# Kernel tuning notes

Measured on AMD Instinct MI355X. Metric: run time of the kernel, lower is better.

The kernel has to match this reference:

```python
import jax, jax.numpy as jnp
import numpy as np

B, S, D, C, K, V = 128, 512, 300, 300, 3, 30000  # batch, seq, embed=hidden, capsule, categories, vocab
PAD_INDEX = 0
SQUASH_EPS = 1e-8
MASK_NEG = -1e9


def squash(x, axis=-1):
    # v * (|v|^2 / (1+|v|^2)) / |v|
    sq = jnp.sum(x * x, axis=axis, keepdims=True)
    return (sq / (1.0 + sq)) * x / jnp.sqrt(sq + SQUASH_EPS)


def setup_inputs() -> dict:
    key = jax.random.key(0)
    ks = jax.random.split(key, 11)
    return {
        "sentence": jax.random.randint(ks[0], (B, S), 0, V),
        "aspect": jax.random.randint(ks[1], (B,), 0, V),
        "category_alpha": jax.random.uniform(ks[2], (B, S), dtype=jnp.float32),
        "embed": jax.random.normal(ks[3], (V, D), dtype=jnp.float32) * 0.02,
        "W_s": jax.random.normal(ks[4], (D, C), dtype=jnp.float32) * 0.02,
        "b_s": jnp.zeros((C,), dtype=jnp.float32),
        "W_a": jax.random.normal(ks[5], (D, C), dtype=jnp.float32) * 0.02,
        "b_a": jnp.zeros((C,), dtype=jnp.float32),
        "W_att": jax.random.normal(ks[6], (C, C), dtype=jnp.float32) * 0.02,
        "guide_capsule": jax.random.normal(ks[7], (K, C), dtype=jnp.float32) * 0.02,
        "guide_weight": jax.random.normal(ks[8], (C, C), dtype=jnp.float32) * 0.02,
        "scale": jnp.asarray(5.0, dtype=jnp.float32),
    }


def reference(sentence, aspect, category_alpha, embed, W_s, b_s, W_a, b_a,
              W_att, guide_capsule, guide_weight, scale):
    mask = sentence != PAD_INDEX                      # [B,S]
    emb = embed[sentence]                             # [B,S,D]
    asp = embed[aspect]                               # [B,D]

    # element_wise_mul (vectorized): per-token alpha weighting
    caml = emb * category_alpha[..., None]            # [B,S,D]
    cavl = jnp.sum(caml, axis=1)                      # [B,D] (unused in non-Cav path)
    del cavl

    # _sentence_encode stand-in (abstract in source): alpha-weighted embeddings
    sent_enc = caml                                   # [B,S,hidden=D]

    primary = squash(sent_enc @ W_s + b_s)            # [B,S,C]
    aspect_capsule = squash(asp @ W_a + b_a)          # [B,C]

    # bilinear attention weights with padding mask, softmax over sequence
    scores = jnp.einsum('bsc,cd,bd->bs', primary, W_att, aspect_capsule)
    scores = jnp.where(mask, scores, MASK_NEG)
    norm_weight = jax.nn.softmax(scores, axis=-1)     # [B,S]

    # capsule-guided routing
    guide = squash(guide_capsule)                     # [K,C]
    gm = jnp.einsum('bsc,cd,kd->bsk', primary, guide_weight, guide)
    gm = jax.nn.softmax(gm, axis=-1) * norm_weight[..., None] * scale
    category_capsule = squash(jnp.einsum('bsk,bsc->bkc', gm, primary))  # [B,K,C]

    return jnp.sqrt(jnp.sum(category_capsule * category_capsule, axis=-1))  # [B,K]
```

## Files before the change

kernel.cpp:

```cpp
#include <hip/hip_runtime.h>

#define NV 30000
#define NB 128
#define NS 512
#define ND 300
#define NC 300
#define CP 304
#define KP 320
#define EP 304
#define MASK_NEG -1e9f
#define SQ_EPS 1e-8f

typedef __attribute__((ext_vector_type(4))) float f32x4;
typedef __attribute__((ext_vector_type(8))) __bf16 bf16x8;

__device__ __forceinline__ unsigned short f2bf(float x){
  unsigned int u = __float_as_uint(x);
  u += 0x7FFFu + ((u >> 16) & 1u);
  return (unsigned short)(u >> 16);
}
__device__ __forceinline__ float bf2f(unsigned short h){
  return __uint_as_float(((unsigned int)h) << 16);
}

__device__ __forceinline__ float bsum512(float v, float* red, int tid){
  red[tid] = v; __syncthreads();
  float s = 0.f;
  if (tid < 64){
    s = red[tid]+red[tid+64]+red[tid+128]+red[tid+192]
      + red[tid+256]+red[tid+320]+red[tid+384]+red[tid+448];
    #pragma unroll
    for (int off = 32; off > 0; off >>= 1) s += __shfl_xor(s, off);
    if (tid == 0) red[0] = s;
  }
  __syncthreads();
  s = red[0];
  __syncthreads();
  return s;
}

__device__ __forceinline__ float bmax512(float v, float* red, int tid){
  red[tid] = v; __syncthreads();
  float s = MASK_NEG;
  if (tid < 64){
    s = red[tid];
    #pragma unroll
    for (int o = 64; o < 512; o += 64) s = fmaxf(s, red[tid+o]);
    #pragma unroll
    for (int off = 32; off > 0; off >>= 1) s = fmaxf(s, __shfl_xor(s, off));
    if (tid == 0) red[0] = s;
  }
  __syncthreads();
  s = red[0];
  __syncthreads();
  return s;
}

__global__ __launch_bounds__(512) void kprep(
    const float* __restrict__ Ws, const float* __restrict__ Watt,
    const float* __restrict__ Gw, const float* __restrict__ bs,
    const float* __restrict__ gcap, const int* __restrict__ aspect,
    const float* __restrict__ embed, const float* __restrict__ Wa,
    const float* __restrict__ ba,
    unsigned short* __restrict__ wt, float* __restrict__ bsp,
    unsigned short* __restrict__ BMT)
{
  int bid = blockIdx.x, tid = threadIdx.x;
  int lane = tid & 63, w = tid >> 6;
  __shared__ float sh[64*65];
  float* aspL = sh;
  float* capL = sh + 320;
  float* red  = sh + 640;

  if (bid < 25) {
    float (*t)[65] = (float(*)[65])sh;
    int kt = bid / 5, nt = bid - kt*5;
    #pragma unroll
    for (int i = 0; i < 8; i++){
      int idx = i*512 + tid;
      int r = idx >> 6, c = idx & 63;
      int gk = kt*64 + r, gn = nt*64 + c;
      t[r][c] = (gk < ND && gn < NC) ? Ws[gk*NC + gn] : 0.f;
    }
    __syncthreads();
    #pragma unroll
    for (int i = 0; i < 8; i++){
      int idx = i*512 + tid;
      int n = idx >> 6, k = idx & 63;
      wt[(nt*64 + n)*KP + kt*64 + k] = f2bf(t[k][n]);
    }
  } else if (bid == 25) {
    float bv = 0.f;
    if (tid < 320){
      bv = (tid < NC) ? bs[tid] : 0.f;
      bsp[tid] = bv;
      BMT[131*KP + tid] = f2bf(bv);
    }
    for (int i = tid; i < 28*KP; i += 512) BMT[132*KP + i] = 0;
  } else if (bid < 154) {
    int b = bid - 26;
    int a = aspect[b];
    if (tid < 320) aspL[tid] = (tid < ND) ? embed[(size_t)a*ND + tid] : 0.f;
    __syncthreads();
    int c = tid;
    float p0=0.f,p1=0.f,p2=0.f,p3=0.f,p4=0.f,p5=0.f;
    if (c < NC){
      for (int d = 0; d < 300; d += 6){
        p0 += Wa[(d+0)*NC + c]*aspL[d+0];
        p1 += Wa[(d+1)*NC + c]*aspL[d+1];
        p2 += Wa[(d+2)*NC + c]*aspL[d+2];
        p3 += Wa[(d+3)*NC + c]*aspL[d+3];
        p4 += Wa[(d+4)*NC + c]*aspL[d+4];
        p5 += Wa[(d+5)*NC + c]*aspL[d+5];
      }
    }
    float z = (c < NC) ? (ba[c] + ((p0+p1)+(p2+p3)+(p4+p5))) : 0.f;
    float sq = bsum512((c < NC) ? z*z : 0.f, red, tid);
    float ssv = (sq/(1.f+sq))/sqrtf(sq + SQ_EPS);
    if (tid < 320) capL[tid] = (c < NC) ? z*ssv : 0.f;
    __syncthreads();
    for (int cc = w; cc < NC; cc += 8){
      const float* wr = Watt + (size_t)cc*NC;
      float acc = 0.f;
      #pragma unroll
      for (int j = 0; j < 5; j++){
        int d = j*64 + lane;
        float wv = (d < ND) ? wr[d] : 0.f;
        acc += wv*capL[d];
      }
      #pragma unroll
      for (int off = 32; off > 0; off >>= 1) acc += __shfl_xor(acc, off);
      if (lane == 0) BMT[(size_t)b*KP + cc] = f2bf(acc);
    }
    if (tid < 20) BMT[(size_t)b*KP + 300 + tid] = 0;
  } else {
    int k = bid - 154;
    if (tid < 320) aspL[tid] = (tid < NC) ? gcap[k*NC + tid] : 0.f;
    __syncthreads();
    float g = (tid < 320) ? aspL[tid] : 0.f;
    float sq = bsum512((tid < NC) ? g*g : 0.f, red, tid);
    float ssv = (sq/(1.f+sq))/sqrtf(sq + SQ_EPS);
    if (tid < 320) capL[tid] = g*ssv;
    __syncthreads();
    for (int cc = w; cc < NC; cc += 8){
      const float* wr = Gw + (size_t)cc*NC;
      float acc = 0.f;
      #pragma unroll
      for (int j = 0; j < 5; j++){
        int d = j*64 + lane;
        float wv = (d < ND) ? wr[d] : 0.f;
        acc += wv*capL[d];
      }
      #pragma unroll
      for (int off = 32; off > 0; off >>= 1) acc += __shfl_xor(acc, off);
      if (lane == 0) BMT[(size_t)(128+k)*KP + cc] = f2bf(acc);
    }
    if (tid < 20) BMT[(size_t)(128+k)*KP + 300 + tid] = 0;
  }
}

#define BM 64
#define BKT 64
#define LDK 72
#define LDE 328
__global__ __launch_bounds__(512) void k1f(
    const float* __restrict__ embed, const unsigned short* __restrict__ wt,
    const unsigned short* __restrict__ BMT, const float* __restrict__ bsp,
    unsigned short* __restrict__ E, float* __restrict__ EtT,
    float* __restrict__ ETS)
{
  __shared__ unsigned short lds_a[BM*LDK];
  __shared__ unsigned short lds_b[KP*LDK];
  __shared__ float e2part[4][BM];
  int tid = threadIdx.x;
  int lane = tid & 63, wid = tid >> 6;
  int bid = blockIdx.x;
  bool special = (bid == (NV + BM - 1)/BM);
  int rowbase = special ? NV : bid * BM;
  unsigned short* et = lds_b;

  if (!special){
    int wrow = wid >> 2, wcol = wid & 3;
    f32x4 acc[2][5];
    f32x4 zero = {0.f,0.f,0.f,0.f};
    #pragma unroll
    for (int m = 0; m < 2; m++)
      #pragma unroll
      for (int n = 0; n < 5; n++) acc[m][n] = zero;

    for (int k0 = 0; k0 < KP; k0 += BKT){
      #pragma unroll
      for (int r = 0; r < 2; r++){
        int id = r*512 + tid;
        int row = id >> 4, k4 = (id & 15) << 2;
        int gk = k0 + k4, grow = rowbase + row;
        float4 v = {0.f,0.f,0.f,0.f};
        if (grow < NV && gk < ND) v = *(const float4*)(embed + (size_t)grow*ND + gk);
        unsigned int lo = (unsigned int)f2bf(v.x) | ((unsigned int)f2bf(v.y) << 16);
        unsigned int hi = (unsigned int)f2bf(v.z) | ((unsigned int)f2bf(v.w) << 16);
        uint2 pk; pk.x = lo; pk.y = hi;
        *(uint2*)(lds_a + row*LDK + k4) = pk;
      }
      #pragma unroll
      for (int r = 0; r < 5; r++){
        int id = r*512 + tid;
        int n = id >> 3, koff = (id & 7) << 3;
        uint4 v = *(const uint4*)(wt + n*KP + k0 + koff);
        *(uint4*)(lds_b + n*LDK + koff) = v;
      }
      __syncthreads();
      #pragma unroll
      for (int kk = 0; kk < BKT; kk += 32){
        bf16x8 af[2], bfr[5];
        int kidx = kk + (lane >> 4)*8;
        int arow = wrow*32 + (lane & 15);
        int brow = wcol*80 + (lane & 15);
        #pragma unroll
        for (int m = 0; m < 2; m++) af[m] = *(const bf16x8*)(lds_a + (arow + m*16)*LDK + kidx);
        #pragma unroll
        for (int n = 0; n < 5; n++) bfr[n] = *(const bf16x8*)(lds_b + (brow + n*16)*LDK + kidx);
        #pragma unroll
        for (int m = 0; m < 2; m++)
          #pragma unroll
          for (int n = 0; n < 5; n++)
            acc[m][n] = __builtin_amdgcn_mfma_f32_16x16x32_bf16(af[m], bfr[n], acc[m][n], 0, 0, 0);
      }
      __syncthreads();
    }
    int colb = wcol*80 + (lane & 15);
    int rowb0 = wrow*32 + ((lane >> 4) << 2);
    #pragma unroll
    for (int m = 0; m < 2; m++)
      #pragma unroll
      for (int n = 0; n < 5; n++)
        #pragma unroll
        for (int j = 0; j < 4; j++){
          int rloc = rowb0 + m*16 + j;
          int row = rowbase + rloc;
          int col = colb + n*16;
          unsigned short h = f2bf(acc[m][n][j]);
          if (row < NV && col < EP) E[(size_t)row*EP + col] = h;
          et[rloc*LDE + col] = h;
        }
    #pragma unroll
    for (int m = 0; m < 2; m++)
      #pragma unroll
      for (int j = 0; j < 4; j++){
        float p = 0.f;
        #pragma unroll
        for (int n = 0; n < 5; n++){ float t = acc[m][n][j]; p += t*t; }
        #pragma unroll
        for (int off = 1; off < 16; off <<= 1) p += __shfl_xor(p, off);
        if ((lane & 15) == 0)
          e2part[wcol][rowb0 + m*16 + j] = p;
      }
  } else {
    for (int i = tid; i < 64*LDE; i += 512) et[i] = 0;
    if (tid < 320) et[tid] = f2bf(bsp[tid]);
  }
  __syncthreads();
  if (!special && tid < BM){
    int grow = rowbase + tid;
    if (grow < NV){
      float s = e2part[0][tid] + e2part[1][tid] + e2part[2][tid] + e2part[3][tid];
      ETS[(size_t)grow*8 + 4] = s;
    }
  }
  int wr2 = wid >> 1, wc2 = wid & 1;
  f32x4 acc2[5];
  f32x4 z2 = {0.f,0.f,0.f,0.f};
  #pragma unroll
  for (int n = 0; n < 5; n++) acc2[n] = z2;
  #pragma unroll 2
  for (int kk = 0; kk < KP; kk += 32){
    int kidx = kk + (lane >> 4)*8;
    bf16x8 a2 = *(const bf16x8*)(et + (wr2*16 + (lane & 15))*LDE + kidx);
    #pragma unroll
    for (int n = 0; n < 5; n++){
      bf16x8 b2 = *(const bf16x8*)(BMT + (size_t)(wc2*80 + n*16 + (lane & 15))*KP + kidx);
      acc2[n] = __builtin_amdgcn_mfma_f32_16x16x32_bf16(a2, b2, acc2[n], 0, 0, 0);
    }
  }
  int colb2 = wc2*80 + (lane & 15);
  int rowb2 = rowbase + wr2*16 + ((lane >> 4) << 2);
  int rlim = special ? (NV + 1) : NV;
  #pragma unroll
  for (int n = 0; n < 5; n++)
    #pragma unroll
    for (int j = 0; j < 4; j++){
      int row = rowb2 + j;
      int col = colb2 + n*16;
      if (row < rlim){
        if (col < 128)      EtT[(size_t)row*128 + col] = acc2[n][j];
        else if (col < 132) ETS[(size_t)row*8 + (col - 128)] = acc2[n][j];
      }
    }
}

__global__ __launch_bounds__(512) void k45(
    const int* __restrict__ sentence, const float* __restrict__ alpha,
    const float* __restrict__ scale_p, const unsigned short* __restrict__ E,
    const float* __restrict__ EtT, const float* __restrict__ ETS,
    const float* __restrict__ bsp, float* __restrict__ out)
{
  int b = blockIdx.x, tid = threadIdx.x;
  int lane = tid & 63, w = tid >> 6;
  __shared__ float red[512];
  __shared__ float cfs[NS*3];
  __shared__ int toksh[NS];
  __shared__ float cap8[8][3][CP];
  __shared__ float vall[3*CP];

  int idx = (b << 9) + tid;
  int tok = sentence[idx];
  float al = alpha[idx];
  toksh[tid] = tok;
  float et  = EtT[(size_t)tok*128 + b];
  float4 eg = *(const float4*)(ETS + (size_t)tok*8);
  float e2v = ETS[(size_t)tok*8 + 4];
  float bst = EtT[(size_t)NV*128 + b];
  float4 brs = *(const float4*)(ETS + (size_t)NV*8);

  float sq  = al*al*e2v + 2.f*al*eg.w + brs.w;
  float ssv = (sq/(1.f+sq))/sqrtf(sq + SQ_EPS);
  float scv = (tok != 0) ? ssv*(al*et + bst) : MASK_NEG;
  float u0 = ssv*(al*eg.x + brs.x);
  float u1 = ssv*(al*eg.y + brs.y);
  float u2 = ssv*(al*eg.z + brs.z);

  float m = bmax512(scv, red, tid);
  float e = expf(scv - m);
  float Z = bsum512(e, red, tid);
  float nw = e / Z;
  float mk = fmaxf(u0, fmaxf(u1, u2));
  float e0 = expf(u0-mk), e1 = expf(u1-mk), e2 = expf(u2-mk);
  float wf = nw * scale_p[0] / (e0+e1+e2);
  float w0 = e0*wf, w1 = e1*wf, w2 = e2*wf;
  float ca = ssv * al;
  cfs[tid*3+0] = w0*ca; cfs[tid*3+1] = w1*ca; cfs[tid*3+2] = w2*ca;
  float sb0 = bsum512(w0*ssv, red, tid);
  float sb1 = bsum512(w1*ssv, red, tid);
  float sb2 = bsum512(w2*ssv, red, tid);
  __syncthreads();

  f32x4 A0 = {0.f,0.f,0.f,0.f}, A1 = A0, A2 = A0, R0 = A0, R1 = A0, R2 = A0;
  int c0 = lane << 2;
  int c1 = 256 + (lane << 2);
  bool rem = lane < 12;
  int base = w << 6;
  #pragma unroll 4
  for (int i = 0; i < 64; i++){
    int s = base + i;
    int t = toksh[s];
    const unsigned short* erow = E + (size_t)t*EP;
    uint2 ev = *(const uint2*)(erow + c0);
    float cf0 = cfs[s*3+0], cf1 = cfs[s*3+1], cf2 = cfs[s*3+2];
    f32x4 y;
    y[0] = bf2f((unsigned short)(ev.x & 0xffffu));
    y[1] = bf2f((unsigned short)(ev.x >> 16));
    y[2] = bf2f((unsigned short)(ev.y & 0xffffu));
    y[3] = bf2f((unsigned short)(ev.y >> 16));
    A0 += cf0*y; A1 += cf1*y; A2 += cf2*y;
    if (rem){
      uint2 ev2 = *(const uint2*)(erow + c1);
      f32x4 yr;
      yr[0] = bf2f((unsigned short)(ev2.x & 0xffffu));
      yr[1] = bf2f((unsigned short)(ev2.x >> 16));
      yr[2] = bf2f((unsigned short)(ev2.y & 0xffffu));
      yr[3] = bf2f((unsigned short)(ev2.y >> 16));
      R0 += cf0*yr; R1 += cf1*yr; R2 += cf2*yr;
    }
  }
  *(f32x4*)&cap8[w][0][c0] = A0;
  *(f32x4*)&cap8[w][1][c0] = A1;
  *(f32x4*)&cap8[w][2][c0] = A2;
  if (rem){
    *(f32x4*)&cap8[w][0][c1] = R0;
    *(f32x4*)&cap8[w][1][c1] = R1;
    *(f32x4*)&cap8[w][2][c1] = R2;
  }
  __syncthreads();
  float sbk[3] = {sb0, sb1, sb2};
  for (int p = tid; p < 3*CP; p += 512){
    int k = p / CP, c = p - k*CP;
    float v = sbk[k]*bsp[c];
    #pragma unroll
    for (int w8 = 0; w8 < 8; w8++) v += cap8[w8][k][c];
    vall[p] = v;
  }
  __syncthreads();
  #pragma unroll
  for (int k = 0; k < 3; k++){
    float x = 0.f;
    if (tid < CP){ float t = vall[k*CP + tid]; x = t*t; }
    float s = bsum512(x, red, tid);
    if (tid == 0){
      out[b*3 + k] = (s/(1.f+s))*sqrtf(s)/sqrtf(s + SQ_EPS);
    }
  }
}

extern "C" void kernel_launch(void* const* d_in, const int* in_sizes, int n_in,
                              void* d_out, int out_size, void* d_ws, size_t ws_size,
                              hipStream_t stream)
{
  (void)in_sizes; (void)n_in; (void)out_size; (void)ws_size;
  const int*   sentence = (const int*)d_in[0];
  const int*   aspect   = (const int*)d_in[1];
  const float* alpha    = (const float*)d_in[2];
  const float* embed    = (const float*)d_in[3];
  const float* Ws       = (const float*)d_in[4];
  const float* bs       = (const float*)d_in[5];
  const float* Wa       = (const float*)d_in[6];
  const float* ba       = (const float*)d_in[7];
  const float* Watt     = (const float*)d_in[8];
  const float* gcap     = (const float*)d_in[9];
  const float* gw       = (const float*)d_in[10];
  const float* scale    = (const float*)d_in[11];
  float* out = (float*)d_out;

  char* w = (char*)d_ws;
  auto alloc = [&](size_t bytes)->char*{
    char* p = w; w += (bytes + 255) & ~(size_t)255; return p;
  };
  unsigned short* WT  = (unsigned short*)alloc((size_t)KP*KP*2);
  unsigned short* E   = (unsigned short*)alloc((size_t)NV*EP*2);
  float* ETT = (float*)alloc((size_t)(NV+1)*128*4);
  float* ETS = (float*)alloc((size_t)(NV+1)*8*4);
  float* BSP = (float*)alloc(320*4);
  unsigned short* BMT = (unsigned short*)alloc((size_t)160*KP*2);

  kprep<<<157, 512, 0, stream>>>(Ws, Watt, gw, bs, gcap, aspect, embed, Wa, ba,
                                 WT, BSP, BMT);
  k1f<<<(NV + BM - 1)/BM + 1, 512, 0, stream>>>(embed, WT, BMT, BSP, E, ETT, ETS);
  k45<<<NB, 512, 0, stream>>>(sentence, alpha, scale, E, ETT, ETS, BSP, out);
}
```

Baseline: 112.3 us.

## Fold attention/guide projections into combined weight and defer Ws projection to end

New measurement: 120.4 us. 7.2% more time.

```diff
diff --git a/kernel.cpp b/kernel.cpp
--- a/kernel.cpp
+++ b/kernel.cpp
@@ -7,20 +7,21 @@
 #define NC 300
 #define CP 304
 #define KP 320
-#define EP 304
 #define MASK_NEG -1e9f
 #define SQ_EPS 1e-8f
 
 typedef __attribute__((ext_vector_type(4))) float f32x4;
 typedef __attribute__((ext_vector_type(8))) __bf16 bf16x8;
 
-__device__ __forceinline__ unsigned short f2bf(float x){
+__device__ __forceinline__ unsigned int f2bfu(float x){
   unsigned int u = __float_as_uint(x);
   u += 0x7FFFu + ((u >> 16) & 1u);
-  return (unsigned short)(u >> 16);
-}
-__device__ __forceinline__ float bf2f(unsigned short h){
-  return __uint_as_float(((unsigned int)h) << 16);
+  return u >> 16;
+}
+__device__ __forceinline__ unsigned short f2bf(float x){ return (unsigned short)f2bfu(x); }
+
+__device__ __forceinline__ int swzk(int row, int k){
+  return (k & ~0x38) | (((((k >> 3) & 7) ^ (row & 7)) & 7) << 3);
 }
 
 __device__ __forceinline__ float bsum512(float v, float* red, int tid){
@@ -62,15 +63,15 @@
     const float* __restrict__ gcap, const int* __restrict__ aspect,
     const float* __restrict__ embed, const float* __restrict__ Wa,
     const float* __restrict__ ba,
-    unsigned short* __restrict__ wt, float* __restrict__ bsp,
-    unsigned short* __restrict__ BMT)
+    unsigned short* __restrict__ WTC, float* __restrict__ BC)
 {
   int bid = blockIdx.x, tid = threadIdx.x;
   int lane = tid & 63, w = tid >> 6;
   __shared__ float sh[64*65];
-  float* aspL = sh;
+  float* vecL = sh;
   float* capL = sh + 320;
-  float* red  = sh + 640;
+  float* tL   = sh + 640;
+  float* red  = sh + 960;
 
   if (bid < 25) {
     float (*t)[65] = (float(*)[65])sh;
@@ -87,40 +88,56 @@
     for (int i = 0; i < 8; i++){
       int idx = i*512 + tid;
       int n = idx >> 6, k = idx & 63;
-      wt[(nt*64 + n)*KP + kt*64 + k] = f2bf(t[k][n]);
+      int row = nt*64 + n, gk = kt*64 + k;
+      WTC[row*KP + swzk(row, gk)] = f2bf(t[k][n]);
     }
   } else if (bid == 25) {
-    float bv = 0.f;
-    if (tid < 320){
-      bv = (tid < NC) ? bs[tid] : 0.f;
-      bsp[tid] = bv;
-      BMT[131*KP + tid] = f2bf(bv);
-    }
-    for (int i = tid; i < 28*KP; i += 512) BMT[132*KP + i] = 0;
-  } else if (bid < 154) {
-    int b = bid - 26;
+    for (int i = tid; i < 60*KP; i += 512) WTC[452*KP + i] = 0;
+    float bv = (tid < NC) ? bs[tid] : 0.f;
+    float s2 = bsum512(bv*bv, red, tid);
+    if (tid == 0) BC[131] = s2;
+  } else if (bid == 26) {
+    if (tid < 320) vecL[tid] = (tid < NC) ? bs[tid] : 0.f;
+    __syncthreads();
+    for (int d = w; d < 320; d += 8){
+      float acc = 0.f;
+      if (d < ND){
+        const float* wr = Ws + (size_t)d*NC;
+        #pragma unroll
+        for (int j = 0; j < 5; j++){
+          int c = j*64 + lane;
+          float wv = (c < NC) ? wr[c] : 0.f;
+          acc += wv*vecL[c];
+        }
+        #pragma unroll
+        for (int off = 32; off > 0; off >>= 1) acc += __shfl_xor(acc, off);
+      }
+      if (lane == 0) WTC[451*KP + swzk(451, d)] = (d < ND) ? f2bf(acc) : (unsigned short)0;
+    }
+  } else if (bid < 155) {
+    int b = bid - 27;
     int a = aspect[b];
-    if (tid < 320) aspL[tid] = (tid < ND) ? embed[(size_t)a*ND + tid] : 0.f;
-    __syncthreads();
-    int c = tid;
-    float p0=0.f,p1=0.f,p2=0.f,p3=0.f,p4=0.f,p5=0.f;
-    if (c < NC){
+    if (tid < 320) vecL[tid] = (tid < ND) ? embed[(size_t)a*ND + tid] : 0.f;
+    __syncthreads();
+    float z = 0.f;
+    if (tid < NC){
+      float p0=0.f,p1=0.f,p2=0.f,p3=0.f,p4=0.f,p5=0.f;
       for (int d = 0; d < 300; d += 6){
-        p0 += Wa[(d+0)*NC + c]*aspL[d+0];
-        p1 += Wa[(d+1)*NC + c]*aspL[d+1];
-        p2 += Wa[(d+2)*NC + c]*aspL[d+2];
-        p3 += Wa[(d+3)*NC + c]*aspL[d+3];
-        p4 += Wa[(d+4)*NC + c]*aspL[d+4];
-        p5 += Wa[(d+5)*NC + c]*aspL[d+5];
-      }
-    }
-    float z = (c < NC) ? (ba[c] + ((p0+p1)+(p2+p3)+(p4+p5))) : 0.f;
-    float sq = bsum512((c < NC) ? z*z : 0.f, red, tid);
+        p0 += Wa[(d+0)*NC + tid]*vecL[d+0];
+        p1 += Wa[(d+1)*NC + tid]*vecL[d+1];
+        p2 += Wa[(d+2)*NC + tid]*vecL[d+2];
+        p3 += Wa[(d+3)*NC + tid]*vecL[d+3];
+        p4 += Wa[(d+4)*NC + tid]*vecL[d+4];
+        p5 += Wa[(d+5)*NC + tid]*vecL[d+5];
+      }
+      z = ba[tid] + ((p0+p1)+(p2+p3)+(p4+p5));
+    }
+    float sq = bsum512((tid < NC) ? z*z : 0.f, red, tid);
     float ssv = (sq/(1.f+sq))/sqrtf(sq + SQ_EPS);
-    if (tid < 320) capL[tid] = (c < NC) ? z*ssv : 0.f;
-    __syncthreads();
-    for (int cc = w; cc < NC; cc += 8){
-      const float* wr = Watt + (size_t)cc*NC;
+    if (tid < 320) capL[tid] = (tid < NC) ? z*ssv : 0.f;
+    __syncthreads();
+    for (int c = w; c < NC; c += 8){
+      const float* wr = Watt + (size_t)c*NC;
       float acc = 0.f;
       #pragma unroll
       for (int j = 0; j < 5; j++){
@@ -130,20 +147,39 @@
       }
       #pragma unroll
       for (int off = 32; off > 0; off >>= 1) acc += __shfl_xor(acc, off);
-      if (lane == 0) BMT[(size_t)b*KP + cc] = f2bf(acc);
-    }
-    if (tid < 20) BMT[(size_t)b*KP + 300 + tid] = 0;
+      if (lane == 0) tL[c] = acc;
+    }
+    __syncthreads();
+    if (tid < 20) tL[300 + tid] = 0.f;
+    float bst = bsum512((tid < NC) ? bs[tid]*tL[tid] : 0.f, red, tid);
+    if (tid == 0) BC[b] = bst;
+    int row = 320 + b;
+    for (int d = w; d < 320; d += 8){
+      float acc = 0.f;
+      if (d < ND){
+        const float* wr = Ws + (size_t)d*NC;
+        #pragma unroll
+        for (int j = 0; j < 5; j++){
+          int c = j*64 + lane;
+          float wv = (c < NC) ? wr[c] : 0.f;
+          acc += wv*tL[c];
+        }
+        #pragma unroll
+        for (int off = 32; off > 0; off >>= 1) acc += __shfl_xor(acc, off);
+      }
+      if (lane == 0) WTC[row*KP + swzk(row, d)] = (d < ND) ? f2bf(acc) : (unsigned short)0;
+    }
   } else {
-    int k = bid - 154;
-    if (tid < 320) aspL[tid] = (tid < NC) ? gcap[k*NC + tid] : 0.f;
-    __syncthreads();
-    float g = (tid < 320) ? aspL[tid] : 0.f;
+    int k = bid - 155;
+    if (tid < 320) vecL[tid] = (tid < NC) ? gcap[k*NC + tid] : 0.f;
+    __syncthreads();
+    float g = (tid < 320) ? vecL[tid] : 0.f;
     float sq = bsum512((tid < NC) ? g*g : 0.f, red, tid);
     float ssv = (sq/(1.f+sq))/sqrtf(sq + SQ_EPS);
     if (tid < 320) capL[tid] = g*ssv;
     __syncthreads();
-    for (int cc = w; cc < NC; cc += 8){
-      const float* wr = Gw + (size_t)cc*NC;
+    for (int c = w; c < NC; c += 8){
+      const float* wr = Gw + (size_t)c*NC;
       float acc = 0.f;
       #pragma unroll
       for (int j = 0; j < 5; j++){
@@ -153,222 +189,218 @@
       }
       #pragma unroll
       for (int off = 32; off > 0; off >>= 1) acc += __shfl_xor(acc, off);
-      if (lane == 0) BMT[(size_t)(128+k)*KP + cc] = f2bf(acc);
-    }
-    if (tid < 20) BMT[(size_t)(128+k)*KP + 300 + tid] = 0;
-  }
-}
-
-#define BM 64
-#define BKT 64
+      if (lane == 0) tL[c] = acc;
+    }
+    __syncthreads();
+    if (tid < 20) tL[300 + tid] = 0.f;
+    float bsg = bsum512((tid < NC) ? bs[tid]*tL[tid] : 0.f, red, tid);
+    if (tid == 0) BC[128 + k] = bsg;
+    int row = 448 + k;
+    for (int d = w; d < 320; d += 8){
+      float acc = 0.f;
+      if (d < ND){
+        const float* wr = Ws + (size_t)d*NC;
+        #pragma unroll
+        for (int j = 0; j < 5; j++){
+          int c = j*64 + lane;
+          float wv = (c < NC) ? wr[c] : 0.f;
+          acc += wv*tL[c];
+        }
+        #pragma unroll
+        for (int off = 32; off > 0; off >>= 1) acc += __shfl_xor(acc, off);
+      }
+      if (lane == 0) WTC[row*KP + swzk(row, d)] = (d < ND) ? f2bf(acc) : (unsigned short)0;
+    }
+  }
+}
+
 #define LDK 72
-#define LDE 328
-__global__ __launch_bounds__(512) void k1f(
-    const float* __restrict__ embed, const unsigned short* __restrict__ wt,
-    const unsigned short* __restrict__ BMT, const float* __restrict__ bsp,
-    unsigned short* __restrict__ E, float* __restrict__ EtT,
-    float* __restrict__ ETS)
+__global__ __launch_bounds__(512, 4) void k1f(
+    const float* __restrict__ embed, const unsigned short* __restrict__ WTC,
+    float* __restrict__ EtT, float* __restrict__ ETS)
 {
-  __shared__ unsigned short lds_a[BM*LDK];
-  __shared__ unsigned short lds_b[KP*LDK];
-  __shared__ float e2part[4][BM];
-  int tid = threadIdx.x;
-  int lane = tid & 63, wid = tid >> 6;
+  __shared__ unsigned short lds_a[64*LDK];
+  __shared__ unsigned short lds_b[512*64];
+  __shared__ float e2part[3][64];
+  int tid = threadIdx.x, lane = tid & 63, wid = tid >> 6;
+  int wrow = wid >> 2, wcol = wid & 3;
+  int rowbase = blockIdx.x * 64;
+  f32x4 acc[2][8];
+  f32x4 zero = {0.f,0.f,0.f,0.f};
+  #pragma unroll
+  for (int m = 0; m < 2; m++)
+    #pragma unroll
+    for (int n = 0; n < 8; n++) acc[m][n] = zero;
+
+  float4 pa[2];
+  auto loadA = [&](int k0){
+    #pragma unroll
+    for (int r = 0; r < 2; r++){
+      int id = r*512 + tid;
+      int row = id >> 4, k4 = (id & 15) << 2;
+      int grow = rowbase + row, gk = k0 + k4;
+      float4 v = {0.f,0.f,0.f,0.f};
+      if (grow < NV && gk < ND) v = *(const float4*)(embed + (size_t)grow*ND + gk);
+      pa[r] = v;
+    }
+  };
+  auto writeA = [&](){
+    #pragma unroll
+    for (int r = 0; r < 2; r++){
+      int id = r*512 + tid;
+      int row = id >> 4, k4 = (id & 15) << 2;
+      uint2 pk;
+      pk.x = f2bfu(pa[r].x) | (f2bfu(pa[r].y) << 16);
+      pk.y = f2bfu(pa[r].z) | (f2bfu(pa[r].w) << 16);
+      *(uint2*)(lds_a + row*LDK + k4) = pk;
+    }
+  };
+  auto stageB = [&](int k0){
+    uint4 pb[8];
+    #pragma unroll
+    for (int r = 0; r < 8; r++){
+      int id = r*512 + tid;
+      pb[r] = *(const uint4*)(WTC + (size_t)(id >> 3)*KP + k0 + (id & 7)*8);
+    }
+    #pragma unroll
+    for (int r = 0; r < 8; r++){
+      int id = r*512 + tid;
+      *(uint4*)((char*)lds_b + id*16) = pb[r];
+    }
+  };
+
+  loadA(0);
+  writeA();
+  stageB(0);
+  loadA(64);
+  __syncthreads();
+  for (int step = 0; step < 5; step++){
+    #pragma unroll
+    for (int kk = 0; kk < 64; kk += 32){
+      int kidx = kk + (lane >> 4)*8;
+      bf16x8 af[2];
+      #pragma unroll
+      for (int m = 0; m < 2; m++)
+        af[m] = *(const bf16x8*)(lds_a + (wrow*32 + (lane & 15) + m*16)*LDK + kidx);
+      #pragma unroll
+      for (int n = 0; n < 8; n++){
+        int jrow = wcol*128 + n*16 + (lane & 15);
+        int ch = ((kidx >> 3) & 7) ^ (jrow & 7);
+        bf16x8 bv = *(const bf16x8*)((const char*)lds_b + jrow*128 + ch*16);
+        #pragma unroll
+        for (int m = 0; m < 2; m++)
+          acc[m][n] = __builtin_amdgcn_mfma_f32_16x16x32_bf16(af[m], bv, acc[m][n], 0, 0, 0);
+      }
+    }
+    __syncthreads();
+    if (step < 4){
+      writeA();
+      stageB((step+1)*64);
+      if (step < 3) loadA((step+2)*64);
+      __syncthreads();
+    }
+  }
+
+  int rloc = wrow*32 + ((lane >> 4) << 2);
+  #pragma unroll
+  for (int m = 0; m < 2; m++)
+    #pragma unroll
+    for (int n = 0; n < 8; n++){
+      int col = wcol*128 + n*16 + (lane & 15);
+      #pragma unroll
+      for (int j = 0; j < 4; j++){
+        int grow = rowbase + rloc + m*16 + j;
+        if (grow < NV){
+          if (col >= 320 && col < 448)      EtT[(size_t)grow*128 + (col - 320)] = acc[m][n][j];
+          else if (col >= 448 && col < 452) ETS[(size_t)grow*8 + (col - 448)] = acc[m][n][j];
+        }
+      }
+    }
+  #pragma unroll
+  for (int m = 0; m < 2; m++)
+    #pragma unroll
+    for (int j = 0; j < 4; j++){
+      float p = 0.f;
+      #pragma unroll
+      for (int n = 0; n < 8; n++)
+        if (wcol*128 + n*16 < 320){ float t = acc[m][n][j]; p += t*t; }
+      #pragma unroll
+      for (int off = 1; off < 16; off <<= 1) p += __shfl_xor(p, off);
+      if ((lane & 15) == 0 && wcol < 3) e2part[wcol][rloc + m*16 + j] = p;
+    }
+  __syncthreads();
+  if (tid < 64){
+    int grow = rowbase + tid;
+    if (grow < NV)
+      ETS[(size_t)grow*8 + 4] = e2part[0][tid] + e2part[1][tid] + e2part[2][tid];
+  }
+}
+
+__global__ __launch_bounds__(512) void k45a(
+    const int* __restrict__ sentence, const float* __restrict__ alpha,
+    const float* __restrict__ scale_p, const float* __restrict__ embed,
+    const float* __restrict__ EtT, const float* __restrict__ ETS,
+    const float* __restrict__ BC, float* __restrict__ SBB, float* __restrict__ PRT)
+{
   int bid = blockIdx.x;
-  bool special = (bid == (NV + BM - 1)/BM);
-  int rowbase = special ? NV : bid * BM;
-  unsigned short* et = lds_b;
-
-  if (!special){
-    int wrow = wid >> 2, wcol = wid & 3;
-    f32x4 acc[2][5];
-    f32x4 zero = {0.f,0.f,0.f,0.f};
-    #pragma unroll
-    for (int m = 0; m < 2; m++)
-      #pragma unroll
-      for (int n = 0; n < 5; n++) acc[m][n] = zero;
-
-    for (int k0 = 0; k0 < KP; k0 += BKT){
-      #pragma unroll
-      for (int r = 0; r < 2; r++){
-        int id = r*512 + tid;
-        int row = id >> 4, k4 = (id & 15) << 2;
-        int gk = k0 + k4, grow = rowbase + row;
-        float4 v = {0.f,0.f,0.f,0.f};
-        if (grow < NV && gk < ND) v = *(const float4*)(embed + (size_t)grow*ND + gk);
-        unsigned int lo = (unsigned int)f2bf(v.x) | ((unsigned int)f2bf(v.y) << 16);
-        unsigned int hi = (unsigned int)f2bf(v.z) | ((unsigned int)f2bf(v.w) << 16);
-        uint2 pk; pk.x = lo; pk.y = hi;
-        *(uint2*)(lds_a + row*LDK + k4) = pk;
-      }
-      #pragma unroll
-      for (int r = 0; r < 5; r++){
-        int id = r*512 + tid;
-        int n = id >> 3, koff = (id & 7) << 3;
-        uint4 v = *(const uint4*)(wt + n*KP + k0 + koff);
-        *(uint4*)(lds_b + n*LDK + koff) = v;
-      }
-      __syncthreads();
-      #pragma unroll
-      for (int kk = 0; kk < BKT; kk += 32){
-        bf16x8 af[2], bfr[5];
-        int kidx = kk + (lane >> 4)*8;
-        int arow = wrow*32 + (lane & 15);
-        int brow = wcol*80 + (lane & 15);
-        #pragma unroll
-        for (int m = 0; m < 2; m++) af[m] = *(const bf16x8*)(lds_a + (arow + m*16)*LDK + kidx);
-        #pragma unroll
-        for (int n = 0; n < 5; n++) bfr[n] = *(const bf16x8*)(lds_b + (brow + n*16)*LDK + kidx);
-        #pragma unroll
-        for (int m = 0; m < 2; m++)
-          #pragma unroll
-          for (int n = 0; n < 5; n++)
-            acc[m][n] = __builtin_amdgcn_mfma_f32_16x16x32_bf16(af[m], bfr[n], acc[m][n], 0, 0, 0);
-      }
-      __syncthreads();
-    }
-    int colb = wcol*80 + (lane & 15);
-    int rowb0 = wrow*32 + ((lane >> 4) << 2);
-    #pragma unroll
-    for (int m = 0; m < 2; m++)
-      #pragma unroll
-      for (int n = 0; n < 5; n++)
-        #pragma unroll
-        for (int j = 0; j < 4; j++){
-          int rloc = rowb0 + m*16 + j;
-          int row = rowbase + rloc;
-          int col = colb + n*16;
-          unsigned short h = f2bf(acc[m][n][j]);
-          if (row < NV && col < EP) E[(size_t)row*EP + col] = h;
-          et[rloc*LDE + col] = h;
-        }
-    #pragma unroll
-    for (int m = 0; m < 2; m++)
-      #pragma unroll
-      for (int j = 0; j < 4; j++){
-        float p = 0.f;
-        #pragma unroll
-        for (int n = 0; n < 5; n++){ float t = acc[m][n][j]; p += t*t; }
-        #pragma unroll
-        for (int off = 1; off < 16; off <<= 1) p += __shfl_xor(p, off);
-        if ((lane & 15) == 0)
-          e2part[wcol][rowb0 + m*16 + j] = p;
-      }
-  } else {
-    for (int i = tid; i < 64*LDE; i += 512) et[i] = 0;
-    if (tid < 320) et[tid] = f2bf(bsp[tid]);
-  }
-  __syncthreads();
-  if (!special && tid < BM){
-    int grow = rowbase + tid;
-    if (grow < NV){
-      float s = e2part[0][tid] + e2part[1][tid] + e2part[2][tid] + e2part[3][tid];
-      ETS[(size_t)grow*8 + 4] = s;
-    }
-  }
-  int wr2 = wid >> 1, wc2 = wid & 1;
-  f32x4 acc2[5];
-  f32x4 z2 = {0.f,0.f,0.f,0.f};
-  #pragma unroll
-  for (int n = 0; n < 5; n++) acc2[n] = z2;
-  #pragma unroll 2
-  for (int kk = 0; kk < KP; kk += 32){
-    int kidx = kk + (lane >> 4)*8;
-    bf16x8 a2 = *(const bf16x8*)(et + (wr2*16 + (lane & 15))*LDE + kidx);
-    #pragma unroll
-    for (int n = 0; n < 5; n++){
-      bf16x8 b2 = *(const bf16x8*)(BMT + (size_t)(wc2*80 + n*16 + (lane & 15))*KP + kidx);
-      acc2[n] = __builtin_amdgcn_mfma_f32_16x16x32_bf16(a2, b2, acc2[n], 0, 0, 0);
-    }
-  }
-  int colb2 = wc2*80 + (lane & 15);
-  int rowb2 = rowbase + wr2*16 + ((lane >> 4) << 2);
-  int rlim = special ? (NV + 1) : NV;
-  #pragma unroll
-  for (int n = 0; n < 5; n++)
-    #pragma unroll
-    for (int j = 0; j < 4; j++){
-      int row = rowb2 + j;
-      int col = colb2 + n*16;
-      if (row < rlim){
-        if (col < 128)      EtT[(size_t)row*128 + col] = acc2[n][j];
-        else if (col < 132) ETS[(size_t)row*8 + (col - 128)] = acc2[n][j];
-      }
-    }
-}
-
-__global__ __launch_bounds__(512) void k45(
-    const int* __restrict__ sentence, const float* __restrict__ alpha,
-    const float* __restrict__ scale_p, const unsigned short* __restrict__ E,
-    const float* __restrict__ EtT, const float* __restrict__ ETS,
-    const float* __restrict__ bsp, float* __restrict__ out)
-{
-  int b = blockIdx.x, tid = threadIdx.x;
-  int lane = tid & 63, w = tid >> 6;
+  int b = bid >> 1, hb = bid & 1;
+  int tid = threadIdx.x, lane = tid & 63, w = tid >> 6;
   __shared__ float red[512];
   __shared__ float cfs[NS*3];
   __shared__ int toksh[NS];
   __shared__ float cap8[8][3][CP];
-  __shared__ float vall[3*CP];
 
   int idx = (b << 9) + tid;
   int tok = sentence[idx];
   float al = alpha[idx];
   toksh[tid] = tok;
-  float et  = EtT[(size_t)tok*128 + b];
+  float et = EtT[(size_t)tok*128 + b];
   float4 eg = *(const float4*)(ETS + (size_t)tok*8);
-  float e2v = ETS[(size_t)tok*8 + 4];
-  float bst = EtT[(size_t)NV*128 + b];
-  float4 brs = *(const float4*)(ETS + (size_t)NV*8);
-
-  float sq  = al*al*e2v + 2.f*al*eg.w + brs.w;
+  float e2 = ETS[(size_t)tok*8 + 4];
+  float bst = BC[b];
+  float bsg0 = BC[128], bsg1 = BC[129], bsg2 = BC[130], bs2 = BC[131];
+
+  float sq = al*al*e2 + 2.f*al*eg.w + bs2;
   float ssv = (sq/(1.f+sq))/sqrtf(sq + SQ_EPS);
   float scv = (tok != 0) ? ssv*(al*et + bst) : MASK_NEG;
-  float u0 = ssv*(al*eg.x + brs.x);
-  float u1 = ssv*(al*eg.y + brs.y);
-  float u2 = ssv*(al*eg.z + brs.z);
+  float u0 = ssv*(al*eg.x + bsg0);
+  float u1 = ssv*(al*eg.y + bsg1);
+  float u2 = ssv*(al*eg.z + bsg2);
 
   float m = bmax512(scv, red, tid);
   float e = expf(scv - m);
   float Z = bsum512(e, red, tid);
   float nw = e / Z;
   float mk = fmaxf(u0, fmaxf(u1, u2));
-  float e0 = expf(u0-mk), e1 = expf(u1-mk), e2 = expf(u2-mk);
-  float wf = nw * scale_p[0] / (e0+e1+e2);
-  float w0 = e0*wf, w1 = e1*wf, w2 = e2*wf;
+  float e0 = expf(u0-mk), e1 = expf(u1-mk), e2k = expf(u2-mk);
+  float wf = nw * scale_p[0] / (e0+e1+e2k);
+  float w0 = e0*wf, w1 = e1*wf, w2 = e2k*wf;
   float ca = ssv * al;
   cfs[tid*3+0] = w0*ca; cfs[tid*3+1] = w1*ca; cfs[tid*3+2] = w2*ca;
   float sb0 = bsum512(w0*ssv, red, tid);
   float sb1 = bsum512(w1*ssv, red, tid);
   float sb2 = bsum512(w2*ssv, red, tid);
+  if (hb == 0 && tid == 0){ SBB[b*3+0] = sb0; SBB[b*3+1] = sb1; SBB[b*3+2] = sb2; }
   __syncthreads();
 
   f32x4 A0 = {0.f,0.f,0.f,0.f}, A1 = A0, A2 = A0, R0 = A0, R1 = A0, R2 = A0;
   int c0 = lane << 2;
   int c1 = 256 + (lane << 2);
-  bool rem = lane < 12;
-  int base = w << 6;
+  bool rem = lane < 11;
+  int base = (hb << 8) + (w << 5);
   #pragma unroll 4
-  for (int i = 0; i < 64; i++){
+  for (int i = 0; i < 32; i++){
     int s = base + i;
     int t = toksh[s];
-    const unsigned short* erow = E + (size_t)t*EP;
-    uint2 ev = *(const uint2*)(erow + c0);
+    const float* er = embed + (size_t)t*ND;
+    float4 y = *(const float4*)(er + c0);
     float cf0 = cfs[s*3+0], cf1 = cfs[s*3+1], cf2 = cfs[s*3+2];
-    f32x4 y;
-    y[0] = bf2f((unsigned short)(ev.x & 0xffffu));
-    y[1] = bf2f((unsigned short)(ev.x >> 16));
-    y[2] = bf2f((unsigned short)(ev.y & 0xffffu));
-    y[3] = bf2f((unsigned short)(ev.y >> 16));
-    A0 += cf0*y; A1 += cf1*y; A2 += cf2*y;
+    f32x4 yv = {y.x, y.y, y.z, y.w};
+    A0 += cf0*yv; A1 += cf1*yv; A2 += cf2*yv;
     if (rem){
-      uint2 ev2 = *(const uint2*)(erow + c1);
-      f32x4 yr;
-      yr[0] = bf2f((unsigned short)(ev2.x & 0xffffu));
-      yr[1] = bf2f((unsigned short)(ev2.x >> 16));
-      yr[2] = bf2f((unsigned short)(ev2.y & 0xffffu));
-      yr[3] = bf2f((unsigned short)(ev2.y >> 16));
-      R0 += cf0*yr; R1 += cf1*yr; R2 += cf2*yr;
+      float4 y2 = *(const float4*)(er + c1);
+      f32x4 y2v = {y2.x, y2.y, y2.z, y2.w};
+      R0 += cf0*y2v; R1 += cf1*y2v; R2 += cf2*y2v;
     }
   }
   *(f32x4*)&cap8[w][0][c0] = A0;
@@ -380,23 +412,54 @@
     *(f32x4*)&cap8[w][2][c1] = R2;
   }
   __syncthreads();
-  float sbk[3] = {sb0, sb1, sb2};
   for (int p = tid; p < 3*CP; p += 512){
     int k = p / CP, c = p - k*CP;
-    float v = sbk[k]*bsp[c];
-    #pragma unroll
-    for (int w8 = 0; w8 < 8; w8++) v += cap8[w8][k][c];
-    vall[p] = v;
-  }
-  __syncthreads();
-  #pragma unroll
-  for (int k = 0; k < 3; k++){
-    float x = 0.f;
-    if (tid < CP){ float t = vall[k*CP + tid]; x = t*t; }
-    float s = bsum512(x, red, tid);
-    if (tid == 0){
-      out[b*3 + k] = (s/(1.f+s))*sqrtf(s)/sqrtf(s + SQ_EPS);
-    }
+    float v = 0.f;
+    if (c < 300){
+      #pragma unroll
+      for (int w8 = 0; w8 < 8; w8++) v += cap8[w8][k][c];
+    }
+    PRT[((size_t)bid*3 + k)*CP + c] = v;
+  }
+}
+
+__global__ __launch_bounds__(512) void k45b(
+    const float* __restrict__ PRT, const float* __restrict__ SBB,
+    const float* __restrict__ bs, const float* __restrict__ Ws,
+    float* __restrict__ out)
+{
+  int b = blockIdx.x, tid = threadIdx.x;
+  __shared__ float Qs[3][CP];
+  __shared__ float red[512];
+  for (int p = tid; p < 3*CP; p += 512){
+    int k = p / CP, c = p - k*CP;
+    float v = 0.f;
+    if (c < 300)
+      v = PRT[((size_t)(2*b)*3 + k)*CP + c] + PRT[((size_t)(2*b+1)*3 + k)*CP + c];
+    Qs[k][c] = v;
+  }
+  __syncthreads();
+  float v0 = 0.f, v1 = 0.f, v2 = 0.f;
+  if (tid < NC){
+    float a0=0.f,a1=0.f,a2=0.f,b0=0.f,b1=0.f,b2=0.f;
+    for (int d = 0; d < 300; d += 2){
+      float wA = Ws[d*NC + tid], wB = Ws[(d+1)*NC + tid];
+      a0 += wA*Qs[0][d]; b0 += wB*Qs[0][d+1];
+      a1 += wA*Qs[1][d]; b1 += wB*Qs[1][d+1];
+      a2 += wA*Qs[2][d]; b2 += wB*Qs[2][d+1];
+    }
+    float bc = bs[tid];
+    v0 = a0+b0 + SBB[b*3+0]*bc;
+    v1 = a1+b1 + SBB[b*3+1]*bc;
+    v2 = a2+b2 + SBB[b*3+2]*bc;
+  }
+  float s0 = bsum512(v0*v0, red, tid);
+  float s1 = bsum512(v1*v1, red, tid);
+  float s2 = bsum512(v2*v2, red, tid);
+  if (tid == 0){
+    out[b*3+0] = (s0/(1.f+s0))*sqrtf(s0)/sqrtf(s0 + SQ_EPS);
+    out[b*3+1] = (s1/(1.f+s1))*sqrtf(s1)/sqrtf(s1 + SQ_EPS);
+    out[b*3+2] = (s2/(1.f+s2))*sqrtf(s2)/sqrtf(s2 + SQ_EPS);
   }
 }
 
@@ -423,15 +486,15 @@
   auto alloc = [&](size_t bytes)->char*{
     char* p = w; w += (bytes + 255) & ~(size_t)255; return p;
   };
-  unsigned short* WT  = (unsigned short*)alloc((size_t)KP*KP*2);
-  unsigned short* E   = (unsigned short*)alloc((size_t)NV*EP*2);
-  float* ETT = (float*)alloc((size_t)(NV+1)*128*4);
-  float* ETS = (float*)alloc((size_t)(NV+1)*8*4);
-  float* BSP = (float*)alloc(320*4);
-  unsigned short* BMT = (unsigned short*)alloc((size_t)160*KP*2);
-
-  kprep<<<157, 512, 0, stream>>>(Ws, Watt, gw, bs, gcap, aspect, embed, Wa, ba,
-                                 WT, BSP, BMT);
-  k1f<<<(NV + BM - 1)/BM + 1, 512, 0, stream>>>(embed, WT, BMT, BSP, E, ETT, ETS);
-  k45<<<NB, 512, 0, stream>>>(sentence, alpha, scale, E, ETT, ETS, BSP, out);
-}
+  unsigned short* WTC = (unsigned short*)alloc((size_t)512*KP*2);
+  float* ETT = (float*)alloc((size_t)NV*128*4);
+  float* ETS = (float*)alloc((size_t)NV*8*4);
+  float* BC  = (float*)alloc(132*4);
+  float* SBB = (float*)alloc(NB*3*4);
+  float* PRT = (float*)alloc((size_t)256*3*CP*4);
+
+  kprep<<<158, 512, 0, stream>>>(Ws, Watt, gw, bs, gcap, aspect, embed, Wa, ba, WTC, BC);
+  k1f<<<(NV + 63)/64, 512, 0, stream>>>(embed, WTC, ETT, ETS);
+  k45a<<<256, 512, 0, stream>>>(sentence, alpha, scale, embed, ETT, ETS, BC, SBB, PRT);
+  k45b<<<NB, 512, 0, stream>>>(PRT, SBB, bs, Ws, out);
+}
```
